# Kernel optimization log

Measured on AMD Instinct MI355X. Metric: run time of the kernel, lower is better.

The kernel has to match this reference:

```python
import jax, jax.numpy as jnp
import numpy as np

B, HW, ENC, E, D, A, V, L = 64, 14, 2048, 512, 512, 512, 32000, 32
LN_EPS = 1e-5


def setup_inputs() -> dict:
    key = jax.random.key(0)
    ks = jax.random.split(key, 16)
    s = 0.02
    n = lambda k, sh: jax.random.normal(k, sh, jnp.float32)
    encoder_out = n(ks[0], (B, HW, HW, ENC))
    encoded_captions = jax.random.randint(ks[1], (B, L), 0, V)
    caption_lengths = jax.random.randint(ks[2], (B, 1), 2, L + 1)
    caption_lengths = caption_lengths.at[0, 0].set(L)  # ensure max length present
    return dict(
        encoder_out=encoder_out,
        encoded_captions=encoded_captions,
        caption_lengths=caption_lengths,
        emb=n(ks[3], (V, E)) * s,
        W_enc_att=n(ks[4], (A, ENC)) * s, b_enc_att=jnp.zeros((A,)),
        W_dec_att=n(ks[5], (A, D)) * s, b_dec_att=jnp.zeros((A,)),
        W_full_att=n(ks[6], (1, A)) * s, b_full_att=jnp.zeros((1,)),
        W_ih=n(ks[7], (4 * D, E + ENC)) * s, b_ih=jnp.zeros((4 * D,)),
        W_hh=n(ks[8], (4 * D, D)) * s, b_hh=jnp.zeros((4 * D,)),
        g_h=jnp.ones((D,)), be_h=jnp.zeros((D,)),
        g_c=jnp.ones((D,)), be_c=jnp.zeros((D,)),
        W_init_h=n(ks[9], (D, ENC)) * s, b_init_h=jnp.zeros((D,)),
        W_init_c=n(ks[10], (D, ENC)) * s, b_init_c=jnp.zeros((D,)),
        W_beta=n(ks[11], (ENC, D)) * s, b_beta=jnp.zeros((ENC,)),
        W_fc=n(ks[12], (V, D)) * s, b_fc=jnp.zeros((V,)),
    )


def _layer_norm(x, g, b):
    m = x.mean(-1, keepdims=True)
    v = ((x - m) ** 2).mean(-1, keepdims=True)
    return (x - m) / jnp.sqrt(v + LN_EPS) * g + b


def reference(encoder_out, encoded_captions, caption_lengths, emb,
              W_enc_att, b_enc_att, W_dec_att, b_dec_att, W_full_att, b_full_att,
              W_ih, b_ih, W_hh, b_hh, g_h, be_h, g_c, be_c,
              W_init_h, b_init_h, W_init_c, b_init_c, W_beta, b_beta, W_fc, b_fc):
    bsz = encoder_out.shape[0]
    enc_out = encoder_out.reshape(bsz, -1, encoder_out.shape[-1])  # [B,P,ENC]
    lengths = caption_lengths[:, 0]
    order = jnp.argsort(-lengths)  # stable descending sort (matches torch sort)
    lengths = lengths[order]
    enc_out = enc_out[order]
    caps = encoded_captions[order]
    embeds = emb[caps]  # [B,L,E]
    decode_lengths = lengths - 1
    T = caps.shape[1] - 1  # static max(decode_lengths)

    mean_enc = enc_out.mean(axis=1)
    h = _layer_norm(mean_enc @ W_init_h.T + b_init_h, g_h, be_h)
    c = _layer_norm(mean_enc @ W_init_c.T + b_init_c, g_c, be_c)

    att1 = enc_out @ W_enc_att.T + b_enc_att  # [B,P,A] precomputed once
    prev_seq = jnp.swapaxes(embeds[:, :T], 0, 1)  # [T,B,E] teacher-forced inputs
    masks = jnp.arange(T)[:, None] < decode_lengths[None, :]  # [T,B] active rows

    def step(carry, xs):
        h, c = carry
        prev, mask = xs
        # attention
        att2 = h @ W_dec_att.T + b_dec_att  # [B,A]
        e = jax.nn.relu(att1 + att2[:, None, :]) @ W_full_att[0] + b_full_att[0]  # [B,P]
        alpha = jax.nn.softmax(e, axis=1)
        awe = jnp.einsum('bpe,bp->be', enc_out, alpha)  # [B,ENC]
        gate = jax.nn.sigmoid(h @ W_beta.T + b_beta)
        awe = gate * awe
        # LSTM cell
        x = jnp.concatenate([prev, awe], axis=1)  # [B,E+ENC]
        gates = x @ W_ih.T + b_ih + h @ W_hh.T + b_hh
        i, f, g, o = jnp.split(gates, 4, axis=1)
        c_new = jax.nn.sigmoid(f) * c + jax.nn.sigmoid(i) * jnp.tanh(g)
        h_new = jax.nn.sigmoid(o) * jnp.tanh(c_new)
        h_new = _layer_norm(h_new, g_h, be_h)
        c_new = _layer_norm(c_new, g_c, be_c)
        preds = h_new @ W_fc.T + b_fc  # [B,V]; dropout is identity in eval
        m = mask[:, None]
        h = jnp.where(m, h_new, h)  # freeze finished rows (== torch batch shrink)
        c = jnp.where(m, c_new, c)
        return (h, c), (jnp.where(m, preds, 0.0), jnp.where(m, alpha, 0.0))

    (_, _), (preds_t, alphas_t) = jax.lax.scan(step, (h, c), (prev_seq, masks))
    predictions = jnp.swapaxes(preds_t, 0, 1)  # [B,T,V]
    alphas = jnp.swapaxes(alphas_t, 0, 1)      # [B,T,P]
    return predictions, caps, decode_lengths, alphas, order
```

## Files before the change

### kernel.cpp

```cpp
#include <hip/hip_runtime.h>
#include <cfloat>
#include <math.h>

#define B_ 64
#define P_ 196
#define ENC_ 2048
#define D_ 512
#define V_ 32000
#define L_ 32
#define T_ 31

#define OUT_PREDS 0L
#define OUT_CAPS  63488000L
#define OUT_DECL  63490048L
#define OUT_ALPH  63490112L
#define OUT_ORDER 63878976L

typedef __bf16 bf16;
typedef __bf16 bf16x8 __attribute__((ext_vector_type(8)));
typedef __bf16 bf16x4 __attribute__((ext_vector_type(4)));
typedef __bf16 bf16x2 __attribute__((ext_vector_type(2)));
typedef float  f32x4  __attribute__((ext_vector_type(4)));

static __device__ __forceinline__ float sigmoidf_(float x) { return 1.f / (1.f + __expf(-x)); }

__global__ void k_order(const int* __restrict__ cap_len, const int* __restrict__ caps,
                        int* __restrict__ order_i, int* __restrict__ declen_i,
                        int* __restrict__ caps_i, float* __restrict__ out,
                        int* __restrict__ rmap, int* __restrict__ orow, int* __restrict__ mact)
{
    __shared__ int len_s[B_], dl_s[B_];
    int tid = threadIdx.x;
    len_s[tid] = cap_len[tid];
    __syncthreads();
    int li = len_s[tid];
    int pos = 0;
    for (int j = 0; j < B_; ++j) {
        int lj = len_s[j];
        pos += (lj > li) || (lj == li && j < tid);
    }
    order_i[pos]  = tid;
    declen_i[pos] = li - 1;
    dl_s[pos]     = li - 1;
    out[OUT_ORDER + pos] = (float)tid;
    out[OUT_DECL  + pos] = (float)(li - 1);
    for (int l = 0; l < L_; ++l) {
        int tok = caps[tid * L_ + l];
        caps_i[pos * L_ + l] = tok;
        out[OUT_CAPS + pos * L_ + l] = (float)tok;
    }
    __syncthreads();
    int p = tid;
    int off = 0;
    for (int j = 0; j < p; ++j) off += dl_s[j];
    int dl = dl_s[p];
    for (int tt = 0; tt < dl; ++tt) {
        rmap[off + tt] = tt * B_ + p;
        orow[off + tt] = p * T_ + tt;
    }
    if (p == B_ - 1) {
        int M = off + dl;
        mact[0] = M;
        int Mr = (M + 63) & ~63;
        for (int i = M; i < Mr; ++i) { rmap[i] = 0; orow[i] = -1; }
    }
}

struct CvtSegs { const float* s[8]; bf16* d[8]; long cum[9]; };
__global__ __launch_bounds__(256) void k_cvt_all(CvtSegs cs)
{
    long i8 = ((long)blockIdx.x * 256 + threadIdx.x) * 8;
    if (i8 >= cs.cum[8]) return;
    int k = 0;
    while (i8 >= cs.cum[k + 1]) ++k;
    long loc = i8 - cs.cum[k];
    const float* src = cs.s[k] + loc;
    float4 a = *(const float4*)(src);
    float4 b = *(const float4*)(src + 4);
    bf16x8 v;
    v[0]=(bf16)a.x; v[1]=(bf16)a.y; v[2]=(bf16)a.z; v[3]=(bf16)a.w;
    v[4]=(bf16)b.x; v[5]=(bf16)b.y; v[6]=(bf16)b.z; v[7]=(bf16)b.w;
    *(bf16x8*)(cs.d[k] + loc) = v;
}

__global__ __launch_bounds__(256) void k_cvt_enc(const float* __restrict__ enc,
                                                 const int* __restrict__ order_i,
                                                 bf16* __restrict__ enc_s)
{
    long i = ((long)blockIdx.x * 256 + threadIdx.x) * 8;
    int b = (int)(i / ((long)P_ * ENC_));
    long rem = i - (long)b * P_ * ENC_;
    const float* src = enc + (long)order_i[b] * P_ * ENC_ + rem;
    float4 a = *(const float4*)(src);
    float4 c = *(const float4*)(src + 4);
    bf16x8 v;
    v[0]=(bf16)a.x; v[1]=(bf16)a.y; v[2]=(bf16)a.z; v[3]=(bf16)a.w;
    v[4]=(bf16)c.x; v[5]=(bf16)c.y; v[6]=(bf16)c.z; v[7]=(bf16)c.w;
    *(bf16x8*)(enc_s + i) = v;
}

__global__ __launch_bounds__(256) void k_meanb(const bf16* __restrict__ enc_s, bf16* __restrict__ mean_b)
{
    int b = blockIdx.x, col = blockIdx.y * 256 + threadIdx.x;
    float s = 0.f;
    const bf16* eb = enc_s + (long)b * P_ * ENC_ + col;
    for (int p = 0; p < P_; ++p) s += (float)eb[(long)p * ENC_];
    mean_b[(long)b * ENC_ + col] = (bf16)(s * (1.f / (float)P_));
}

template<int MI, int FUSE, int EPI, int SWZ>
__global__ void __launch_bounds__(256)
k_mgemm(const bf16* __restrict__ A, long lda,
        const bf16* __restrict__ B1, const bf16* __restrict__ B2,
        const float* __restrict__ bias,
        float* __restrict__ Cf, bf16* __restrict__ Cb,
        int N, int K, int kspl, int Nsp, int Ksp)
{
    const int tid = threadIdx.x;
    const int lane = tid & 63, w = tid >> 6;
    int mt, nt, z;
    if (SWZ == 0) { mt = blockIdx.x; nt = blockIdx.y; z = blockIdx.z; }
    else          { int o = blockIdx.x; int wg = (o & 7) * 49 + (o >> 3);
                    mt = wg >> 2; nt = wg & 3; z = 0; }
    const int krange = K / kspl;
    const int k0 = z * krange, k1 = k0 + krange;
    const int r16 = lane & 15, kq = lane >> 4;
    const int koff = kq * 8;

    const bf16* Ap = A + (long)(mt * (MI * 16) + r16) * lda + koff;
    const int ncol0 = nt * 128 + w * 32;

    const bf16* Bp[2];
    const bf16* B2p[2];
#pragma unroll
    for (int ni = 0; ni < 2; ++ni) {
        int n = ncol0 + ni * 16 + r16;
        if (FUSE == 1)
            Bp[ni] = (n < Nsp) ? B1 + (long)n * K + koff
                               : B2 + (long)(n - Nsp) * K + koff;
        else if (FUSE == 2) {
            Bp[ni]  = B1 + (long)n * Ksp + koff;
            B2p[ni] = B2 + (long)n * (K - Ksp) + koff - Ksp;
        } else
            Bp[ni] = B1 + (long)n * K + koff;
    }

    auto loadA = [&](int kk, bf16x8* dst) {
#pragma unroll
        for (int mi = 0; mi < MI; ++mi)
            dst[mi] = *(const bf16x8*)(Ap + (long)mi * 16 * lda + kk);
    };
    auto loadB = [&](int kk, bf16x8* dst) {
#pragma unroll
        for (int ni = 0; ni < 2; ++ni) {
            if (FUSE == 2 && kk >= Ksp) dst[ni] = *(const bf16x8*)(B2p[ni] + kk);
            else                        dst[ni] = *(const bf16x8*)(Bp[ni] + kk);
        }
    };

    f32x4 acc[MI][2] = {};
    bf16x8 af[MI], bfr[2];
    loadA(k0, af); loadB(k0, bfr);
    for (int kk = k0 + 32; kk < k1; kk += 32) {
        bf16x8 af2[MI], bf2[2];
        loadA(kk, af2); loadB(kk, bf2);
#pragma unroll
        for (int mi = 0; mi < MI; ++mi)
#pragma unroll
            for (int ni = 0; ni < 2; ++ni)
                acc[mi][ni] = __builtin_amdgcn_mfma_f32_16x16x32_bf16(bfr[ni], af[mi], acc[mi][ni], 0, 0, 0);
#pragma unroll
        for (int mi = 0; mi < MI; ++mi) af[mi] = af2[mi];
#pragma unroll
        for (int ni = 0; ni < 2; ++ni) bfr[ni] = bf2[ni];
    }
#pragma unroll
    for (int mi = 0; mi < MI; ++mi)
#pragma unroll
        for (int ni = 0; ni < 2; ++ni)
            acc[mi][ni] = __builtin_amdgcn_mfma_f32_16x16x32_bf16(bfr[ni], af[mi], acc[mi][ni], 0, 0, 0);

#pragma unroll
    for (int mi = 0; mi < MI; ++mi) {
        const int row = mt * (MI * 16) + mi * 16 + r16;
#pragma unroll
        for (int ni = 0; ni < 2; ++ni) {
            const int col = ncol0 + ni * 16 + kq * 4;
            f32x4 v = acc[mi][ni];
            if (EPI == 0) {
                *(f32x4*)(Cf + (long)z * 64 * N + (long)row * N + col) = v;
            } else {
                f32x4 bv = *(const f32x4*)(bias + col);
                bf16x4 o;
                o[0]=(bf16)(v[0]+bv[0]); o[1]=(bf16)(v[1]+bv[1]);
                o[2]=(bf16)(v[2]+bv[2]); o[3]=(bf16)(v[3]+bv[3]);
                *(bf16x4*)(Cb + (long)row * N + col) = o;
            }
        }
    }
}

__global__ __launch_bounds__(512)
void k_initln(const float* __restrict__ pi,
              const float* __restrict__ b_h, const float* __restrict__ b_c,
              const float* __restrict__ g_h, const float* __restrict__ be_h,
              const float* __restrict__ g_c, const float* __restrict__ be_c,
              bf16* __restrict__ xh, float* __restrict__ cbuf)
{
    int b = blockIdx.x, d = threadIdx.x;
    float yh = pi[(long)b * 1024 + d]       + b_h[d];
    float yc = pi[(long)b * 1024 + 512 + d] + b_c[d];
    __shared__ float r1[512], r2[512], r3[512], r4[512];
    r1[d] = yh; r2[d] = yh * yh; r3[d] = yc; r4[d] = yc * yc;
    __syncthreads();
    for (int s = 256; s > 0; s >>= 1) {
        if (d < s) { r1[d]+=r1[d+s]; r2[d]+=r2[d+s]; r3[d]+=r3[d+s]; r4[d]+=r4[d+s]; }
        __syncthreads();
    }
    float mh = r1[0] * (1.f/512.f), vh = r2[0] * (1.f/512.f) - mh*mh;
    float mc = r3[0] * (1.f/512.f), vc = r4[0] * (1.f/512.f) - mc*mc;
    float hln = (yh - mh) * rsqrtf(vh + 1e-5f) * g_h[d] + be_h[d];
    float cln = (yc - mc) * rsqrtf(vc + 1e-5f) * g_c[d] + be_c[d];
    xh[(long)b * 3072 + 2560 + d] = (bf16)hln;
    cbuf[(long)b * 512 + d] = cln;
}

__global__ __launch_bounds__(256)
void k_attn(const float* __restrict__ att2gate, const float* __restrict__ b_dec,
            const float* __restrict__ b_beta, const float* __restrict__ Wfull,
            const bf16* __restrict__ att1_b, const bf16* __restrict__ enc_s,
            const int* __restrict__ caps_i, const int* __restrict__ declen_i,
            const float* __restrict__ emb,
            bf16* __restrict__ xh, float* __restrict__ out, int t)
{
    const int b = blockIdx.x >> 2, seg = blockIdx.x & 3, tid = threadIdx.x;
    if (t >= declen_i[b]) {
        if (seg == 1 && tid < P_) out[OUT_ALPH + ((long)b * T_ + t) * P_ + tid] = 0.f;
        return;
    }
    __shared__ float att2s[512], wf[512], red[256], alp[P_];
    for (int i = tid; i < 512; i += 256) {
        float s = b_dec[i];
#pragma unroll
        for (int zz = 0; zz < 4; ++zz) s += att2gate[((long)zz * 64 + b) * 2560 + i];
        att2s[i] = s;
        wf[i] = Wfull[i];
    }
    __syncthreads();
    float ev = -FLT_MAX;
    if (tid < P_) {
        const bf16* ar = att1_b + ((long)b * P_ + tid) * 512;
        float acc = 0.f;
        for (int a0 = 0; a0 < 512; a0 += 8) {
            bf16x8 v = *(const bf16x8*)(ar + a0);
#pragma unroll
            for (int j = 0; j < 8; ++j)
                acc += fmaxf((float)v[j] + att2s[a0 + j], 0.f) * wf[a0 + j];
        }
        ev = acc;
    }
    red[tid] = ev;
    __syncthreads();
    for (int s = 128; s > 0; s >>= 1) { if (tid < s) red[tid] = fmaxf(red[tid], red[tid + s]); __syncthreads(); }
    float mx = red[0];
    __syncthreads();
    float ex = (tid < P_) ? __expf(ev - mx) : 0.f;
    red[tid] = ex;
    __syncthreads();
    for (int s = 128; s > 0; s >>= 1) { if (tid < s) red[tid] += red[tid + s]; __syncthreads(); }
    float inv = 1.f / red[0];
    if (tid < P_) alp[tid] = ex * inv;
    __syncthreads();
    if (seg == 1 && tid < P_)
        out[OUT_ALPH + ((long)b * T_ + t) * P_ + tid] = alp[tid];
    const int c0 = seg * 512 + tid * 2;
    const bf16* eb = enc_s + (long)b * P_ * ENC_ + c0;
    float a0 = 0.f, a1 = 0.f;
#pragma unroll 4
    for (int p = 0; p < P_; ++p) {
        bf16x2 v = *(const bf16x2*)(eb + (long)p * ENC_);
        float al = alp[p];
        a0 += al * (float)v[0]; a1 += al * (float)v[1];
    }
    float g0 = b_beta[c0], g1 = b_beta[c0 + 1];
#pragma unroll
    for (int zz = 0; zz < 4; ++zz) {
        const float* gs = att2gate + ((long)zz * 64 + b) * 2560 + 512 + c0;
        g0 += gs[0]; g1 += gs[1];
    }
    bf16x2 o;
    o[0] = (bf16)(a0 * sigmoidf_(g0));
    o[1] = (bf16)(a1 * sigmoidf_(g1));
    *(bf16x2*)(xh + (long)b * 3072 + 512 + c0) = o;
    if (seg == 0) {
        int tok = caps_i[b * L_ + t];
        for (int i = tid; i < 512; i += 256)
            xh[(long)b * 3072 + i] = (bf16)emb[(long)tok * 512 + i];
    }
}

__global__ __launch_bounds__(512)
void k_lstm(const float* __restrict__ gp, const float* __restrict__ b_ih, const float* __restrict__ b_hh,
            const float* __restrict__ g_h, const float* __restrict__ be_h,
            const float* __restrict__ g_c, const float* __restrict__ be_c,
            bf16* __restrict__ xh, float* __restrict__ cbuf, bf16* __restrict__ hseq,
            const int* __restrict__ declen_i, int t)
{
    int b = blockIdx.x, d = threadIdx.x;
    if (t >= declen_i[b]) return;
    float iv = b_ih[d]        + b_hh[d];
    float fv = b_ih[512 + d]  + b_hh[512 + d];
    float gv = b_ih[1024 + d] + b_hh[1024 + d];
    float ov = b_ih[1536 + d] + b_hh[1536 + d];
#pragma unroll
    for (int s = 0; s < 8; ++s) {
        const float* gs = gp + ((long)s * B_ + b) * 2048;
        iv += gs[d]; fv += gs[512 + d]; gv += gs[1024 + d]; ov += gs[1536 + d];
    }
    float cn = sigmoidf_(fv) * cbuf[(long)b * 512 + d] + sigmoidf_(iv) * tanhf(gv);
    float hn = sigmoidf_(ov) * tanhf(cn);
    __shared__ float r1[512], r2[512], r3[512], r4[512];
    r1[d] = hn; r2[d] = hn * hn; r3[d] = cn; r4[d] = cn * cn;
    __syncthreads();
    for (int s = 256; s > 0; s >>= 1) {
        if (d < s) { r1[d]+=r1[d+s]; r2[d]+=r2[d+s]; r3[d]+=r3[d+s]; r4[d]+=r4[d+s]; }
        __syncthreads();
    }
    float mh = r1[0] * (1.f/512.f), vh = r2[0] * (1.f/512.f) - mh*mh;
    float mc = r3[0] * (1.f/512.f), vc = r4[0] * (1.f/512.f) - mc*mc;
    float hln = (hn - mh) * rsqrtf(vh + 1e-5f) * g_h[d] + be_h[d];
    float cln = (cn - mc) * rsqrtf(vc + 1e-5f) * g_c[d] + be_c[d];
    bf16 hv = (bf16)hln;
    xh[(long)b * 3072 + 2560 + d] = hv;
    hseq[((long)t * B_ + b) * 512 + d] = hv;
    cbuf[(long)b * 512 + d] = cln;
}

__global__ __launch_bounds__(256) void k_zero(const int* __restrict__ declen_i, float* __restrict__ out)
{
    int x = blockIdx.x;
    int b = x / T_, t = x - b * T_;
    if (t < declen_i[b]) return;
    float4 z = {0.f, 0.f, 0.f, 0.f};
    long base = OUT_PREDS + ((long)b * T_ + t) * V_;
    for (int i = threadIdx.x * 4; i < V_; i += 1024)
        *(float4*)(out + base + i) = z;
}

__global__ __launch_bounds__(256)
void k_preds(const bf16* __restrict__ hseq, const bf16* __restrict__ Wfc,
             const float* __restrict__ bias,
             const int* __restrict__ rmap, const int* __restrict__ orow,
             const int* __restrict__ mact, float* __restrict__ out)
{
    int o = blockIdx.x; int xcd = o & 7;
    int base = xcd < 6 ? xcd * 969 : 5814 + (xcd - 6) * 968;
    int wg = base + (o >> 3);
    int nt = wg / 31, mt = wg - 31 * nt;
    if (mt * 64 >= mact[0]) return;
    __shared__ int rs[64], os[64];
    __shared__ __align__(16) float ct[64][132];
    const int tid = threadIdx.x, lane = tid & 63, w = tid >> 6;
    const int r16 = lane & 15, kq = lane >> 4, koff = kq * 8;
    if (tid < 64) { rs[tid] = rmap[mt * 64 + tid]; os[tid] = orow[mt * 64 + tid]; }
    __syncthreads();
    const int ncol0 = nt * 128 + w * 32;
    const bf16* Ap[4];
#pragma unroll
    for (int mi = 0; mi < 4; ++mi)
        Ap[mi] = hseq + (long)rs[mi * 16 + r16] * 512 + koff;
    const bf16* Bp[2];
#pragma unroll
    for (int ni = 0; ni < 2; ++ni)
        Bp[ni] = Wfc + (long)(ncol0 + ni * 16 + r16) * 512 + koff;

    f32x4 acc[4][2] = {};
    bf16x8 af[4], bfr[2];
#pragma unroll
    for (int mi = 0; mi < 4; ++mi) af[mi] = *(const bf16x8*)(Ap[mi]);
#pragma unroll
    for (int ni = 0; ni < 2; ++ni) bfr[ni] = *(const bf16x8*)(Bp[ni]);
    for (int kk = 32; kk < 512; kk += 32) {
        bf16x8 af2[4], bf2[2];
#pragma unroll
        for (int mi = 0; mi < 4; ++mi) af2[mi] = *(const bf16x8*)(Ap[mi] + kk);
#pragma unroll
        for (int ni = 0; ni < 2; ++ni) bf2[ni] = *(const bf16x8*)(Bp[ni] + kk);
#pragma unroll
        for (int mi = 0; mi < 4; ++mi)
#pragma unroll
            for (int ni = 0; ni < 2; ++ni)
                acc[mi][ni] = __builtin_amdgcn_mfma_f32_16x16x32_bf16(bfr[ni], af[mi], acc[mi][ni], 0, 0, 0);
#pragma unroll
        for (int mi = 0; mi < 4; ++mi) af[mi] = af2[mi];
#pragma unroll
        for (int ni = 0; ni < 2; ++ni) bfr[ni] = bf2[ni];
    }
#pragma unroll
    for (int mi = 0; mi < 4; ++mi)
#pragma unroll
        for (int ni = 0; ni < 2; ++ni)
            acc[mi][ni] = __builtin_amdgcn_mfma_f32_16x16x32_bf16(bfr[ni], af[mi], acc[mi][ni], 0, 0, 0);

#pragma unroll
    for (int mi = 0; mi < 4; ++mi)
#pragma unroll
        for (int ni = 0; ni < 2; ++ni)
            *(f32x4*)&ct[mi * 16 + r16][w * 32 + ni * 16 + kq * 4] = acc[mi][ni];
    __syncthreads();
    const int r0 = tid >> 5, cc = (tid & 31) * 4;
    const int gcol = nt * 128 + cc;
    f32x4 bv = *(const f32x4*)(bias + gcol);
#pragma unroll
    for (int it = 0; it < 8; ++it) {
        int r = it * 8 + r0;
        int orv = os[r];
        if (orv >= 0) {
            f32x4 v = *(f32x4*)&ct[r][cc];
            f32x4 oo;
            oo[0] = v[0] + bv[0]; oo[1] = v[1] + bv[1];
            oo[2] = v[2] + bv[2]; oo[3] = v[3] + bv[3];
            *(f32x4*)(out + OUT_PREDS + (long)orv * V_ + gcol) = oo;
        }
    }
}

extern "C" void kernel_launch(void* const* d_in, const int* in_sizes, int n_in,
                              void* d_out, int out_size, void* d_ws, size_t ws_size,
                              hipStream_t stream)
{
    const float* enc       = (const float*)d_in[0];
    const int*   caps      = (const int*)  d_in[1];
    const int*   caplen    = (const int*)  d_in[2];
    const float* emb       = (const float*)d_in[3];
    const float* W_enc_att = (const float*)d_in[4];
    const float* b_enc_att = (const float*)d_in[5];
    const float* W_dec_att = (const float*)d_in[6];
    const float* b_dec_att = (const float*)d_in[7];
    const float* W_full    = (const float*)d_in[8];
    const float* W_ih      = (const float*)d_in[10];
    const float* b_ih      = (const float*)d_in[11];
    const float* W_hh      = (const float*)d_in[12];
    const float* b_hh      = (const float*)d_in[13];
    const float* g_h       = (const float*)d_in[14];
    const float* be_h      = (const float*)d_in[15];
    const float* g_c       = (const float*)d_in[16];
    const float* be_c      = (const float*)d_in[17];
    const float* W_init_h  = (const float*)d_in[18];
    const float* b_init_h  = (const float*)d_in[19];
    const float* W_init_c  = (const float*)d_in[20];
    const float* b_init_c  = (const float*)d_in[21];
    const float* W_beta    = (const float*)d_in[22];
    const float* b_beta    = (const float*)d_in[23];
    const float* W_fc      = (const float*)d_in[24];
    const float* b_fc      = (const float*)d_in[25];
    float* out = (float*)d_out;

    char* w = (char*)d_ws;
    auto alloc = [&](size_t bytes) { char* p = w; w += (bytes + 255) & ~(size_t)255; return p; };
    int*   order_i  = (int*)  alloc(B_ * 4);
    int*   declen_i = (int*)  alloc(B_ * 4);
    int*   caps_i   = (int*)  alloc(B_ * L_ * 4);
    int*   rmap     = (int*)  alloc(2048 * 4);
    int*   orow     = (int*)  alloc(2048 * 4);
    int*   mact     = (int*)  alloc(256);
    bf16*  enc_s    = (bf16*) alloc((size_t)B_ * P_ * ENC_ * 2);
    bf16*  mean_b   = (bf16*) alloc((size_t)B_ * ENC_ * 2);
    bf16*  att1_b   = (bf16*) alloc((size_t)B_ * P_ * 512 * 2);
    float* pi       = (float*)alloc((size_t)B_ * 1024 * 4);
    float* att2gate = (float*)alloc((size_t)4 * B_ * 2560 * 4);
    bf16*  xh       = (bf16*) alloc((size_t)B_ * 3072 * 2);
    float* gp       = (float*)alloc((size_t)8 * B_ * 2048 * 4);
    float* cbuf     = (float*)alloc((size_t)B_ * 512 * 4);
    bf16*  hseq     = (bf16*) alloc((size_t)T_ * B_ * 512 * 2);
    bf16*  W_enc_b  = (bf16*) alloc((size_t)512 * 2048 * 2);
    bf16*  W_dec_b  = (bf16*) alloc((size_t)512 * 512 * 2);
    bf16*  W_beta_b = (bf16*) alloc((size_t)2048 * 512 * 2);
    bf16*  W_ih_b   = (bf16*) alloc((size_t)2048 * 2560 * 2);
    bf16*  W_hh_b   = (bf16*) alloc((size_t)2048 * 512 * 2);
    bf16*  W_fc_b   = (bf16*) alloc((size_t)32000 * 512 * 2);
    bf16*  W_inh_b  = (bf16*) alloc((size_t)512 * 2048 * 2);
    bf16*  W_inc_b  = (bf16*) alloc((size_t)512 * 2048 * 2);

    k_order<<<1, B_, 0, stream>>>(caplen, caps, order_i, declen_i, caps_i, out, rmap, orow, mact);
    k_cvt_enc<<<12544, 256, 0, stream>>>(enc, order_i, enc_s);
    k_meanb<<<dim3(B_, 8), 256, 0, stream>>>(enc_s, mean_b);

    CvtSegs cs;
    const float* srcs[8] = {W_enc_att, W_dec_att, W_beta, W_ih, W_hh, W_fc, W_init_h, W_init_c};
    bf16* dsts[8] = {W_enc_b, W_dec_b, W_beta_b, W_ih_b, W_hh_b, W_fc_b, W_inh_b, W_inc_b};
    long ns[8] = {512L*2048, 512L*512, 2048L*512, 2048L*2560, 2048L*512, 32000L*512, 512L*2048, 512L*2048};
    long cum = 0;
    for (int i = 0; i < 8; ++i) { cs.s[i] = srcs[i]; cs.d[i] = dsts[i]; cs.cum[i] = cum; cum += ns[i]; }
    cs.cum[8] = cum;
    k_cvt_all<<<(int)((cum / 8 + 255) / 256), 256, 0, stream>>>(cs);

    k_mgemm<4, 1, 0, 0><<<dim3(1, 8, 1), 256, 0, stream>>>(mean_b, 2048, W_inh_b, W_inc_b,
        nullptr, pi, nullptr, 1024, 2048, 1, 512, 0);
    k_initln<<<B_, 512, 0, stream>>>(pi, b_init_h, b_init_c, g_h, be_h, g_c, be_c, xh, cbuf);

    k_mgemm<8, 0, 1, 1><<<392, 256, 0, stream>>>(enc_s, 2048, W_enc_b, nullptr,
        b_enc_att, nullptr, att1_b, 512, 2048, 1, 0, 0);

    for (int t = 0; t < T_; ++t) {
        k_mgemm<4, 1, 0, 0><<<dim3(1, 20, 4), 256, 0, stream>>>(xh + 2560, 3072, W_dec_b, W_beta_b,
            nullptr, att2gate, nullptr, 2560, 512, 4, 512, 0);
        k_attn<<<256, 256, 0, stream>>>(att2gate, b_dec_att, b_beta, W_full, att1_b, enc_s,
            caps_i, declen_i, emb, xh, out, t);
        k_mgemm<4, 2, 0, 0><<<dim3(1, 16, 8), 256, 0, stream>>>(xh, 3072, W_ih_b, W_hh_b,
            nullptr, gp, nullptr, 2048, 3072, 8, 0, 2560);
        k_lstm<<<B_, 512, 0, stream>>>(gp, b_ih, b_hh, g_h, be_h, g_c, be_c,
            xh, cbuf, hseq, declen_i, t);
    }

    k_zero<<<B_ * T_, 256, 0, stream>>>(declen_i, out);
    k_preds<<<7750, 256, 0, stream>>>(hseq, W_fc_b, b_fc, rmap, orow, mact, out);
}
```

Before: 2.265 ms.

## Split-K the att1 encoder GEMM with a reduction kernel and halve attention blocks

The one-off encoder attention projection GEMM now uses MI=4 tiles with a 2-way K split, launching 1568 blocks instead of 392. Each block writes fp32 partials, and a new k_red kernel sums the two halves, adds the bias and converts to bf16. The partial buffer is aliased with the gp, att2gate and hseq workspaces. Separately, k_attn now runs 128 blocks of 512 threads instead of 256 blocks of 256, so the per-batch score and softmax work is repeated by 2 blocks rather than 4. The cost is an extra fp32 write and read pass for the partials, plus fewer blocks in the per-step attention kernel.

```diff
diff --git a/kernel.cpp b/kernel.cpp
--- a/kernel.cpp
+++ b/kernel.cpp
@@ -114,14 +114,14 @@
         const bf16* __restrict__ B1, const bf16* __restrict__ B2,
         const float* __restrict__ bias,
         float* __restrict__ Cf, bf16* __restrict__ Cb,
-        int N, int K, int kspl, int Nsp, int Ksp)
+        int N, int K, int kspl, int Nsp, int Ksp, int Mtot)
 {
     const int tid = threadIdx.x;
     const int lane = tid & 63, w = tid >> 6;
     int mt, nt, z;
     if (SWZ == 0) { mt = blockIdx.x; nt = blockIdx.y; z = blockIdx.z; }
-    else          { int o = blockIdx.x; int wg = (o & 7) * 49 + (o >> 3);
-                    mt = wg >> 2; nt = wg & 3; z = 0; }
+    else          { int o = blockIdx.x; int wg = (o & 7) * 196 + (o >> 3);
+                    mt = wg >> 3; nt = (wg >> 1) & 3; z = wg & 1; }
     const int krange = K / kspl;
     const int k0 = z * krange, k1 = k0 + krange;
     const int r16 = lane & 15, kq = lane >> 4;
@@ -188,7 +188,7 @@
             const int col = ncol0 + ni * 16 + kq * 4;
             f32x4 v = acc[mi][ni];
             if (EPI == 0) {
-                *(f32x4*)(Cf + (long)z * 64 * N + (long)row * N + col) = v;
+                *(f32x4*)(Cf + (long)z * Mtot * N + (long)row * N + col) = v;
             } else {
                 f32x4 bv = *(const f32x4*)(bias + col);
                 bf16x4 o;
@@ -200,6 +200,26 @@
     }
 }
 
+__global__ __launch_bounds__(256)
+void k_red(const float* __restrict__ p, const float* __restrict__ bias, bf16* __restrict__ ob)
+{
+    const long TOT = (long)12544 * 512;
+    long i = ((long)blockIdx.x * 256 + threadIdx.x) * 8;
+    f32x4 a0 = *(const f32x4*)(p + i);
+    f32x4 a1 = *(const f32x4*)(p + i + 4);
+    f32x4 b0 = *(const f32x4*)(p + TOT + i);
+    f32x4 b1 = *(const f32x4*)(p + TOT + i + 4);
+    int col = (int)(i & 511);
+    f32x4 c0 = *(const f32x4*)(bias + col);
+    f32x4 c1 = *(const f32x4*)(bias + col + 4);
+    bf16x8 v;
+    v[0]=(bf16)(a0[0]+b0[0]+c0[0]); v[1]=(bf16)(a0[1]+b0[1]+c0[1]);
+    v[2]=(bf16)(a0[2]+b0[2]+c0[2]); v[3]=(bf16)(a0[3]+b0[3]+c0[3]);
+    v[4]=(bf16)(a1[0]+b1[0]+c1[0]); v[5]=(bf16)(a1[1]+b1[1]+c1[1]);
+    v[6]=(bf16)(a1[2]+b1[2]+c1[2]); v[7]=(bf16)(a1[3]+b1[3]+c1[3]);
+    *(bf16x8*)(ob + i) = v;
+}
+
 __global__ __launch_bounds__(512)
 void k_initln(const float* __restrict__ pi,
               const float* __restrict__ b_h, const float* __restrict__ b_c,
@@ -225,7 +245,7 @@
     cbuf[(long)b * 512 + d] = cln;
 }
 
-__global__ __launch_bounds__(256)
+__global__ __launch_bounds__(512)
 void k_attn(const float* __restrict__ att2gate, const float* __restrict__ b_dec,
             const float* __restrict__ b_beta, const float* __restrict__ Wfull,
             const bf16* __restrict__ att1_b, const bf16* __restrict__ enc_s,
@@ -233,18 +253,18 @@
             const float* __restrict__ emb,
             bf16* __restrict__ xh, float* __restrict__ out, int t)
 {
-    const int b = blockIdx.x >> 2, seg = blockIdx.x & 3, tid = threadIdx.x;
+    const int b = blockIdx.x >> 1, seg = blockIdx.x & 1, tid = threadIdx.x;
     if (t >= declen_i[b]) {
         if (seg == 1 && tid < P_) out[OUT_ALPH + ((long)b * T_ + t) * P_ + tid] = 0.f;
         return;
     }
-    __shared__ float att2s[512], wf[512], red[256], alp[P_];
-    for (int i = tid; i < 512; i += 256) {
-        float s = b_dec[i];
-#pragma unroll
-        for (int zz = 0; zz < 4; ++zz) s += att2gate[((long)zz * 64 + b) * 2560 + i];
-        att2s[i] = s;
-        wf[i] = Wfull[i];
+    __shared__ float att2s[512], wf[512], red[512], alp[P_];
+    {
+        float s = b_dec[tid];
+#pragma unroll
+        for (int zz = 0; zz < 4; ++zz) s += att2gate[((long)zz * 64 + b) * 2560 + tid];
+        att2s[tid] = s;
+        wf[tid] = Wfull[tid];
     }
     __syncthreads();
     float ev = -FLT_MAX;
@@ -261,19 +281,19 @@
     }
     red[tid] = ev;
     __syncthreads();
-    for (int s = 128; s > 0; s >>= 1) { if (tid < s) red[tid] = fmaxf(red[tid], red[tid + s]); __syncthreads(); }
+    for (int s = 256; s > 0; s >>= 1) { if (tid < s) red[tid] = fmaxf(red[tid], red[tid + s]); __syncthreads(); }
     float mx = red[0];
     __syncthreads();
     float ex = (tid < P_) ? __expf(ev - mx) : 0.f;
     red[tid] = ex;
     __syncthreads();
-    for (int s = 128; s > 0; s >>= 1) { if (tid < s) red[tid] += red[tid + s]; __syncthreads(); }
+    for (int s = 256; s > 0; s >>= 1) { if (tid < s) red[tid] += red[tid + s]; __syncthreads(); }
     float inv = 1.f / red[0];
     if (tid < P_) alp[tid] = ex * inv;
     __syncthreads();
     if (seg == 1 && tid < P_)
         out[OUT_ALPH + ((long)b * T_ + t) * P_ + tid] = alp[tid];
-    const int c0 = seg * 512 + tid * 2;
+    const int c0 = seg * 1024 + tid * 2;
     const bf16* eb = enc_s + (long)b * P_ * ENC_ + c0;
     float a0 = 0.f, a1 = 0.f;
 #pragma unroll 4
@@ -294,8 +314,7 @@
     *(bf16x2*)(xh + (long)b * 3072 + 512 + c0) = o;
     if (seg == 0) {
         int tok = caps_i[b * L_ + t];
-        for (int i = tid; i < 512; i += 256)
-            xh[(long)b * 3072 + i] = (bf16)emb[(long)tok * 512 + i];
+        xh[(long)b * 3072 + tid] = (bf16)emb[(long)tok * 512 + tid];
     }
 }
 
@@ -468,11 +487,12 @@
     bf16*  mean_b   = (bf16*) alloc((size_t)B_ * ENC_ * 2);
     bf16*  att1_b   = (bf16*) alloc((size_t)B_ * P_ * 512 * 2);
     float* pi       = (float*)alloc((size_t)B_ * 1024 * 4);
-    float* att2gate = (float*)alloc((size_t)4 * B_ * 2560 * 4);
+    float* cbuf     = (float*)alloc((size_t)B_ * 512 * 4);
     bf16*  xh       = (bf16*) alloc((size_t)B_ * 3072 * 2);
-    float* gp       = (float*)alloc((size_t)8 * B_ * 2048 * 4);
-    float* cbuf     = (float*)alloc((size_t)B_ * 512 * 4);
-    bf16*  hseq     = (bf16*) alloc((size_t)T_ * B_ * 512 * 2);
+    float* att1_p   = (float*)alloc((size_t)2 * 12544 * 512 * 4);
+    float* gp       = att1_p;
+    float* att2gate = (float*)((char*)att1_p + ((size_t)8 * B_ * 2048 * 4 + 255 & ~(size_t)255));
+    bf16*  hseq     = (bf16*)((char*)att2gate + ((size_t)4 * B_ * 2560 * 4 + 255 & ~(size_t)255));
     bf16*  W_enc_b  = (bf16*) alloc((size_t)512 * 2048 * 2);
     bf16*  W_dec_b  = (bf16*) alloc((size_t)512 * 512 * 2);
     bf16*  W_beta_b = (bf16*) alloc((size_t)2048 * 512 * 2);
@@ -496,19 +516,20 @@
     k_cvt_all<<<(int)((cum / 8 + 255) / 256), 256, 0, stream>>>(cs);
 
     k_mgemm<4, 1, 0, 0><<<dim3(1, 8, 1), 256, 0, stream>>>(mean_b, 2048, W_inh_b, W_inc_b,
-        nullptr, pi, nullptr, 1024, 2048, 1, 512, 0);
+        nullptr, pi, nullptr, 1024, 2048, 1, 512, 0, 64);
     k_initln<<<B_, 512, 0, stream>>>(pi, b_init_h, b_init_c, g_h, be_h, g_c, be_c, xh, cbuf);
 
-    k_mgemm<8, 0, 1, 1><<<392, 256, 0, stream>>>(enc_s, 2048, W_enc_b, nullptr,
-        b_enc_att, nullptr, att1_b, 512, 2048, 1, 0, 0);
+    k_mgemm<4, 0, 0, 1><<<1568, 256, 0, stream>>>(enc_s, 2048, W_enc_b, nullptr,
+        nullptr, att1_p, nullptr, 512, 2048, 2, 0, 0, 12544);
+    k_red<<<3136, 256, 0, stream>>>(att1_p, b_enc_att, att1_b);
 
     for (int t = 0; t < T_; ++t) {
         k_mgemm<4, 1, 0, 0><<<dim3(1, 20, 4), 256, 0, stream>>>(xh + 2560, 3072, W_dec_b, W_beta_b,
-            nullptr, att2gate, nullptr, 2560, 512, 4, 512, 0);
-        k_attn<<<256, 256, 0, stream>>>(att2gate, b_dec_att, b_beta, W_full, att1_b, enc_s,
+            nullptr, att2gate, nullptr, 2560, 512, 4, 512, 0, 64);
+        k_attn<<<128, 512, 0, stream>>>(att2gate, b_dec_att, b_beta, W_full, att1_b, enc_s,
             caps_i, declen_i, emb, xh, out, t);
         k_mgemm<4, 2, 0, 0><<<dim3(1, 16, 8), 256, 0, stream>>>(xh, 3072, W_ih_b, W_hh_b,
-            nullptr, gp, nullptr, 2048, 3072, 8, 0, 2560);
+            nullptr, gp, nullptr, 2048, 3072, 8, 0, 2560, 64);
         k_lstm<<<B_, 512, 0, stream>>>(gp, b_ih, b_hh, g_h, be_h, g_c, be_c,
             xh, cbuf, hseq, declen_i, t);
     }
```

Result: no change. 2.258 ms (-0.3%).
